# Performance work log

Measured on AMD Instinct MI355X. Metric: run time of the kernel, lower is better.

The kernel has to match this reference:

```python
import jax, jax.numpy as jnp
import numpy as np

EPS = 1e-12
B, S, H, NH, L, F = 8, 512, 768, 12, 12, 3072
V, TV, P = 21128, 2, 512
DH = H // NH


def layer_norm(x, g, b):
    m = jnp.mean(x, axis=-1, keepdims=True)
    v = jnp.var(x, axis=-1, keepdims=True)
    return g * (x - m) / jnp.sqrt(v + EPS) + b


def setup_inputs() -> dict:
    key = jax.random.key(0)
    ks = iter(jax.random.split(key, 40))
    r = lambda shape: (jax.random.normal(next(ks), shape, jnp.float32) * 0.02)
    inp = {
        "input_ids": jax.random.randint(next(ks), (B, S), 0, V, jnp.int32),
        "segment_ids": jax.random.randint(next(ks), (B, S), 0, TV, jnp.int32),
        "attention_mask": jnp.ones((B, 1, 1, S), jnp.float32),
        "tok_emb": r((V, H)),
        "pos_emb": r((P, H)),
        "type_emb": r((TV, H)),
        "emb_g": jnp.ones((H,), jnp.float32),
        "emb_b": jnp.zeros((H,), jnp.float32),
        # stacked per-layer params [L, ...]
        "Wq": r((L, H, H)), "bq": jnp.zeros((L, H), jnp.float32),
        "Wk": r((L, H, H)), "bk": jnp.zeros((L, H), jnp.float32),
        "Wv": r((L, H, H)), "bv": jnp.zeros((L, H), jnp.float32),
        "Wao": r((L, H, H)), "bao": jnp.zeros((L, H), jnp.float32),
        "ln1_g": jnp.ones((L, H), jnp.float32), "ln1_b": jnp.zeros((L, H), jnp.float32),
        "Wi": r((L, H, F)), "bi": jnp.zeros((L, F), jnp.float32),
        "Wio": r((L, F, H)), "bio": jnp.zeros((L, H), jnp.float32),
        "ln2_g": jnp.ones((L, H), jnp.float32), "ln2_b": jnp.zeros((L, H), jnp.float32),
    }
    return inp


def reference(input_ids, segment_ids, attention_mask,
              tok_emb, pos_emb, type_emb, emb_g, emb_b,
              Wq, bq, Wk, bk, Wv, bv, Wao, bao, ln1_g, ln1_b,
              Wi, bi, Wio, bio, ln2_g, ln2_b):
    # ---- embedding: token + type + position, then LayerNorm ----
    x = tok_emb[input_ids] + type_emb[segment_ids] + pos_emb[None, :S, :]
    x = layer_norm(x, emb_g, emb_b)  # [B,S,H]

    mask_add = (1.0 - attention_mask) * -10000.0  # [B,1,1,S]
    scale = 1.0 / jnp.sqrt(jnp.asarray(DH, x.dtype))

    def split_heads(t):  # [B,S,H] -> [B,NH,S,DH]
        return t.reshape(B, S, NH, DH).transpose(0, 2, 1, 3)

    for l in range(Wq.shape[0]):
        q = split_heads(x @ Wq[l] + bq[l])
        k = split_heads(x @ Wk[l] + bk[l])
        v = split_heads(x @ Wv[l] + bv[l])
        score = jnp.einsum("bhqd,bhkd->bhqk", q, k) * scale + mask_add
        attn = jax.nn.softmax(score, axis=-1)
        ctx = jnp.einsum("bhqk,bhkd->bhqd", attn, v)
        ctx = ctx.transpose(0, 2, 1, 3).reshape(B, S, H)
        # attention output: dense + residual + LN
        attn_out = layer_norm(ctx @ Wao[l] + bao[l] + x, ln1_g[l], ln1_b[l])
        # FFN: dense-gelu-dense + residual + LN (exact erf gelu as in tf.keras)
        h = jax.nn.gelu(attn_out @ Wi[l] + bi[l], approximate=False)
        x = layer_norm(h @ Wio[l] + bio[l] + attn_out, ln2_g[l], ln2_b[l])

    return x  # sequence output [B,S,H]
```

## Files before the change

kernel.cpp:

```cpp
#include <hip/hip_runtime.h>
#include <math.h>

static constexpr int Bc = 8;
static constexpr int Sc = 512;
static constexpr int Hc = 768;
static constexpr int NHc = 12;
static constexpr int Lc = 12;
static constexpr int Fc = 3072;
static constexpr int DHc = 64;
static constexpr int NTOK = Bc * Sc;
static constexpr int QKVN = 3 * Hc;

static constexpr size_t W_QKV_OFF = 0;
static constexpr size_t W_AO_OFF  = 1769472;
static constexpr size_t W_I_OFF   = 2359296;
static constexpr size_t W_IO_OFF  = 4718592;
static constexpr size_t LW        = 7077888;

typedef _Float16 h16x8 __attribute__((ext_vector_type(8)));
typedef float f32x4 __attribute__((ext_vector_type(4)));
typedef unsigned short us4 __attribute__((ext_vector_type(4)));
typedef unsigned short us8 __attribute__((ext_vector_type(8)));
typedef unsigned int u32x4 __attribute__((ext_vector_type(4)));

__device__ __forceinline__ unsigned short f2h(float f) {
    _Float16 h = (_Float16)f;
    return __builtin_bit_cast(unsigned short, h);
}
__device__ __forceinline__ float h2f(unsigned short u) {
    return (float)__builtin_bit_cast(_Float16, u);
}

#define AS1 __attribute__((address_space(1)))
#define AS3 __attribute__((address_space(3)))
__device__ __forceinline__ void gld_lds16(const void* g, void* l) {
    __builtin_amdgcn_global_load_lds((const AS1 void*)g, (AS3 void*)l, 16, 0, 0);
}

__global__ __launch_bounds__(256) void prep_kernel(
    const float* __restrict__ Wq, const float* __restrict__ Wk,
    const float* __restrict__ Wv, const float* __restrict__ Wao,
    const float* __restrict__ Wi, const float* __restrict__ Wio,
    const float* __restrict__ bq, const float* __restrict__ bk,
    const float* __restrict__ bv, unsigned short* __restrict__ WALL,
    float* __restrict__ BALL)
{
    int t = blockIdx.x, l = blockIdx.y;
    int tid = threadIdx.x;

    if (t >= 1728) {
        int idx = (t - 1728) * 256 + tid;
        float v = (idx < 768) ? bq[l * Hc + idx]
                : (idx < 1536) ? bk[l * Hc + idx - 768]
                               : bv[l * Hc + idx - 1536];
        BALL[(size_t)l * QKVN + idx] = v;
        return;
    }

    const float* src;
    unsigned short* dst;
    int K, N, ntn, local;
    if (t < 576) {
        int mat = t / 144; local = t % 144;
        K = 768; N = 768; ntn = 12;
        src = (mat == 0 ? Wq : mat == 1 ? Wk : mat == 2 ? Wv : Wao) + (size_t)l * 589824;
        dst = WALL + (size_t)l * LW + (mat < 3 ? (size_t)mat * 589824 : W_AO_OFF);
    } else if (t < 1152) {
        local = t - 576; K = 768; N = 3072; ntn = 48;
        src = Wi + (size_t)l * 2359296;
        dst = WALL + (size_t)l * LW + W_I_OFF;
    } else {
        local = t - 1152; K = 3072; N = 768; ntn = 12;
        src = Wio + (size_t)l * 2359296;
        dst = WALL + (size_t)l * LW + W_IO_OFF;
    }
    int n0 = (local % ntn) * 64, k0 = (local / ntn) * 64;

    int nkt = K >> 6;
    unsigned short* dstb = dst + ((size_t)(n0 >> 7) * nkt + (k0 >> 6)) * 8192
                               + ((n0 >> 6) & 1) * 4096;

    __shared__ float tl[64][65];
    int tx = tid & 15, ty = tid >> 4;
#pragma unroll
    for (int j = 0; j < 4; j++) {
        int k = ty + j * 16;
        float4 v = *(const float4*)(src + (size_t)(k0 + k) * N + n0 + tx * 4);
        tl[k][tx * 4 + 0] = v.x; tl[k][tx * 4 + 1] = v.y;
        tl[k][tx * 4 + 2] = v.z; tl[k][tx * 4 + 3] = v.w;
    }
    __syncthreads();
#pragma unroll
    for (int q = 0; q < 2; q++) {
        int chunk = q * 256 + tid;
        int row = chunk >> 3, c = chunk & 7;
        us8 o;
#pragma unroll
        for (int j = 0; j < 8; j++) o[j] = f2h(tl[c * 8 + j][row]);
        *(us8*)(dstb + (size_t)chunk * 8) = o;
    }
}

__device__ __forceinline__ void ln_stats192(float4 v, float& mean, float& rstd) {
    float s = v.x + v.y + v.z + v.w;
    float s2 = v.x * v.x + v.y * v.y + v.z * v.z + v.w * v.w;
#pragma unroll
    for (int o = 32; o > 0; o >>= 1) { s += __shfl_xor(s, o); s2 += __shfl_xor(s2, o); }
    __shared__ float red[6];
    int lane = threadIdx.x & 63, wid = threadIdx.x >> 6;
    if (lane == 0) { red[wid] = s; red[3 + wid] = s2; }
    __syncthreads();
    float ts  = red[0] + red[1] + red[2];
    float ts2 = red[3] + red[4] + red[5];
    mean = ts * (1.0f / Hc);
    float var = ts2 * (1.0f / Hc) - mean * mean;
    rstd = rsqrtf(var + 1e-12f);
}

__global__ __launch_bounds__(192) void embed_ln_kernel(
    const int* __restrict__ ids, const int* __restrict__ seg,
    const float* __restrict__ tok, const float* __restrict__ typ,
    const float* __restrict__ pos, const float* __restrict__ g,
    const float* __restrict__ b, unsigned short* __restrict__ outb)
{
    int t = blockIdx.x;
    int si = t % Sc;
    int id = ids[t], sg = seg[t];
    int i = threadIdx.x;

    float4 tv = *(const float4*)(tok + (size_t)id * Hc + 4 * i);
    float4 yv = *(const float4*)(typ + (size_t)sg * Hc + 4 * i);
    float4 pv = *(const float4*)(pos + (size_t)si * Hc + 4 * i);
    float4 v = make_float4(tv.x + yv.x + pv.x, tv.y + yv.y + pv.y,
                           tv.z + yv.z + pv.z, tv.w + yv.w + pv.w);
    float mean, rstd;
    ln_stats192(v, mean, rstd);

    float4 gv = *(const float4*)(g + 4 * i);
    float4 bv = *(const float4*)(b + 4 * i);
    us4 ob;
    ob[0] = f2h(gv.x * (v.x - mean) * rstd + bv.x);
    ob[1] = f2h(gv.y * (v.y - mean) * rstd + bv.y);
    ob[2] = f2h(gv.z * (v.z - mean) * rstd + bv.z);
    ob[3] = f2h(gv.w * (v.w - mean) * rstd + bv.w);
    *(us4*)(outb + (size_t)t * Hc + 4 * i) = ob;
}

__global__ __launch_bounds__(192) void add_ln2h_kernel(
    const unsigned short* __restrict__ t0, const unsigned short* __restrict__ t1,
    const unsigned short* __restrict__ res, const float* __restrict__ g,
    const float* __restrict__ b, unsigned short* __restrict__ outb,
    float* __restrict__ outf)
{
    int t = blockIdx.x;
    int i = threadIdx.x;
    us4 a = *(const us4*)(t0 + (size_t)t * Hc + 4 * i);
    us4 c = *(const us4*)(t1 + (size_t)t * Hc + 4 * i);
    us4 r = *(const us4*)(res + (size_t)t * Hc + 4 * i);
    float4 v = make_float4(h2f(a[0]) + h2f(c[0]) + h2f(r[0]),
                           h2f(a[1]) + h2f(c[1]) + h2f(r[1]),
                           h2f(a[2]) + h2f(c[2]) + h2f(r[2]),
                           h2f(a[3]) + h2f(c[3]) + h2f(r[3]));
    float mean, rstd;
    ln_stats192(v, mean, rstd);

    float4 gv = *(const float4*)(g + 4 * i);
    float4 bv = *(const float4*)(b + 4 * i);
    float4 o = make_float4(gv.x * (v.x - mean) * rstd + bv.x,
                           gv.y * (v.y - mean) * rstd + bv.y,
                           gv.z * (v.z - mean) * rstd + bv.z,
                           gv.w * (v.w - mean) * rstd + bv.w);
    us4 ob; ob[0] = f2h(o.x); ob[1] = f2h(o.y); ob[2] = f2h(o.z); ob[3] = f2h(o.w);
    *(us4*)(outb + (size_t)t * Hc + 4 * i) = ob;
    if (outf) *(float4*)(outf + (size_t)t * Hc + 4 * i) = o;
}

template <int OUT>
__global__ __launch_bounds__(256) void gemm_mfma(
    const unsigned short* __restrict__ A,
    const unsigned short* __restrict__ Bt,
    const float* __restrict__ bias,
    unsigned short* __restrict__ Cb,
    unsigned short* __restrict__ VTp,
    int M, int N, int K, int kspan)
{
    __shared__ __align__(16) unsigned short As[128 * 64];
    __shared__ __align__(16) unsigned short Bs[128 * 64];

    int tid = threadIdx.x;
    int l = tid & 63, w = tid >> 6;

    int nbx = gridDim.x;
    int nwg = nbx * gridDim.y;
    int bid = blockIdx.y * nbx + blockIdx.x;
    if ((nwg & 7) == 0) {
        int cpx = nwg >> 3;
        bid = (bid & 7) * cpx + (bid >> 3);
    }
    int m0 = (bid % nbx) * 128, n0 = (bid / nbx) * 128;

    int lr = l & 15;
    int kg = l >> 4;
    int wr = (w >> 1) * 64, wc = (w & 1) * 64;
    int lx = lr & 7;
    int kbeg = blockIdx.z * kspan;
    int nkt = K >> 6;
    const unsigned short* BtRow = Bt + (size_t)(n0 >> 7) * nkt * 8192;

    f32x4 acc[4][4] = {};

    for (int k0 = kbeg; k0 < kbeg + kspan; k0 += 64) {
        const unsigned short* gbBase = BtRow + (size_t)(k0 >> 6) * 8192;
#pragma unroll
        for (int p = 0; p < 4; p++) {
            int i = p * 256 + w * 64 + l;
            int row = i >> 3;
            int slot = (i & 7) ^ (row & 7);
            const unsigned short* ga = A + (size_t)(m0 + row) * K + k0 + slot * 8;
            const unsigned short* gb = gbBase + row * 64 + slot * 8;
            unsigned short* la = As + (size_t)(p * 256 + w * 64) * 8;
            unsigned short* lb = Bs + (size_t)(p * 256 + w * 64) * 8;
            gld_lds16(ga, la);
            gld_lds16(gb, lb);
        }
        asm volatile("s_waitcnt vmcnt(0)" ::: "memory");
        __syncthreads();

#pragma unroll
        for (int kh = 0; kh < 2; kh++) {
            h16x8 av[4], bv[4];
#pragma unroll
            for (int f = 0; f < 4; f++) {
                int sl = (kh * 4 + kg) ^ lx;
                av[f] = *(const h16x8*)(As + (wr + f * 16 + lr) * 64 + sl * 8);
                bv[f] = *(const h16x8*)(Bs + (wc + f * 16 + lr) * 64 + sl * 8);
            }
#pragma unroll
            for (int i = 0; i < 4; i++)
#pragma unroll
                for (int j = 0; j < 4; j++)
                    acc[i][j] = __builtin_amdgcn_mfma_f32_16x16x32_f16(
                        av[i], bv[j], acc[i][j], 0, 0, 0);
        }
        __syncthreads();
    }

#pragma unroll
    for (int i = 0; i < 4; i++) {
        int rbase = m0 + wr + i * 16 + kg * 4;
#pragma unroll
        for (int j = 0; j < 4; j++) {
            int col = n0 + wc + j * 16 + lr;
            float bcol = (OUT == 4 && blockIdx.z > 0) ? 0.f : bias[col];
            if (OUT == 3 && col >= 1536) {
                int vcol = col - 1536;
                int hh = vcol >> 6, d = vcol & 63;
                int bbb = rbase >> 9, s0 = rbase & 511;
                us4 ob;
#pragma unroll
                for (int r = 0; r < 4; r++) ob[r] = f2h(acc[i][j][r] + bcol);
                *(us4*)(VTp + ((((size_t)bbb * NHc + hh) * DHc + d) << 9) + s0) = ob;
            } else if (OUT == 4) {
                unsigned short* op = Cb + (size_t)blockIdx.z * M * N;
#pragma unroll
                for (int r = 0; r < 4; r++)
                    op[(size_t)(rbase + r) * N + col] = f2h(acc[i][j][r] + bcol);
            } else {
                int ldc = (OUT == 3) ? 1536 : N;
#pragma unroll
                for (int r = 0; r < 4; r++) {
                    float v = acc[i][j][r] + bcol;
                    if (OUT == 1) v = 0.5f * v * (1.0f + erff(v * 0.70710678118654752f));
                    Cb[(size_t)(rbase + r) * ldc + col] = f2h(v);
                }
            }
        }
    }
}

__global__ __launch_bounds__(512) void attn_mfma(
    const unsigned short* __restrict__ QK, const unsigned short* __restrict__ VT,
    const float* __restrict__ mask, unsigned short* __restrict__ O)
{
    const int LD = 1536;
    __shared__ __align__(16) unsigned short Ks[64 * 64];
    __shared__ __align__(16) unsigned short Vt[64 * 64];
    __shared__ float Ml[64];

    int tid = threadIdx.x;
    int l = tid & 63, w = tid >> 6;
    int g = l >> 4, c = l & 15;
    int q0 = blockIdx.x * 128;
    int h = blockIdx.y, bb = blockIdx.z;

    const size_t rowQ = (size_t)(bb * Sc + q0 + w * 16 + c) * LD + h * DHc;
    h16x8 qv[2];
    qv[0] = *(const h16x8*)(QK + rowQ + 8 * g);
    qv[1] = *(const h16x8*)(QK + rowQ + 32 + 8 * g);

    float m_run = -1e30f, l_run = 0.f;
    f32x4 acc_o[4] = {};
    const float scale = 0.125f;

    for (int kt = 0; kt < Sc; kt += 64) {
        const unsigned short* Kgb = QK + (size_t)(bb * Sc + kt) * LD + Hc + h * DHc;
        {
            int i = tid;
            int row = i >> 3;
            int slot = (i & 7) ^ (row & 7);
            gld_lds16(Kgb + (size_t)row * LD + slot * 8, Ks + (size_t)(w * 64) * 8);
        }
        const unsigned short* Vg = VT + (((size_t)bb * NHc + h) * DHc << 9) + kt;
        {
            int i = tid;
            int row = i >> 3;
            int slot = (i & 7) ^ (row & 7);
            gld_lds16(Vg + ((size_t)row << 9) + slot * 8, Vt + (size_t)(w * 64) * 8);
        }
        if (tid < 64) Ml[tid] = (1.0f - mask[bb * Sc + kt + tid]) * -10000.0f;
        asm volatile("s_waitcnt vmcnt(0)" ::: "memory");
        __syncthreads();

        f32x4 s[4] = {};
#pragma unroll
        for (int kh = 0; kh < 2; kh++) {
#pragma unroll
            for (int f = 0; f < 4; f++) {
                int row = f * 16 + c;
                h16x8 av = *(const h16x8*)(Ks + row * 64 + (((kh * 4 + g) ^ (row & 7)) * 8));
                s[f] = __builtin_amdgcn_mfma_f32_16x16x32_f16(av, qv[kh], s[f], 0, 0, 0);
            }
        }

        f32x4 mv[4];
#pragma unroll
        for (int f = 0; f < 4; f++) mv[f] = *(const f32x4*)&Ml[f * 16 + 4 * g];
        float mx = -1e30f;
#pragma unroll
        for (int f = 0; f < 4; f++)
#pragma unroll
            for (int r = 0; r < 4; r++) {
                float sv = s[f][r] * scale + mv[f][r];
                s[f][r] = sv;
                mx = fmaxf(mx, sv);
            }
        mx = fmaxf(mx, __shfl_xor(mx, 16));
        mx = fmaxf(mx, __shfl_xor(mx, 32));
        float mn = fmaxf(m_run, mx);
        float fs = __expf(m_run - mn);
        m_run = mn;
        float ps = 0.f;
        f32x4 p[4];
#pragma unroll
        for (int f = 0; f < 4; f++)
#pragma unroll
            for (int r = 0; r < 4; r++) {
                float pv = __expf(s[f][r] - mn);
                p[f][r] = pv;
                ps += pv;
            }
        ps += __shfl_xor(ps, 16);
        ps += __shfl_xor(ps, 32);
        l_run = l_run * fs + ps;
#pragma unroll
        for (int fm = 0; fm < 4; fm++)
#pragma unroll
            for (int r = 0; r < 4; r++) acc_o[fm][r] *= fs;

        unsigned pk[4][2];
#pragma unroll
        for (int f = 0; f < 4; f++)
#pragma unroll
            for (int rp = 0; rp < 2; rp++)
                pk[f][rp] = ((unsigned)f2h(p[f][2 * rp + 1]) << 16) | f2h(p[f][2 * rp]);

#pragma unroll
        for (int kh = 0; kh < 2; kh++) {
            u32x4 bw;
#pragma unroll
            for (int t = 0; t < 4; t++) {
                int srcl = (2 * ((l >> 4) & 1) + (t >> 1)) * 16 + c;
                unsigned lo = __shfl(pk[2 * kh][t & 1], srcl);
                unsigned hi = __shfl(pk[2 * kh + 1][t & 1], srcl);
                bw[t] = (g & 2) ? hi : lo;
            }
            h16x8 bfrag = __builtin_bit_cast(h16x8, bw);
#pragma unroll
            for (int fm = 0; fm < 4; fm++) {
                int row = fm * 16 + c;
                h16x8 av = *(const h16x8*)(Vt + row * 64 + (((kh * 4 + g) ^ (row & 7)) * 8));
                acc_o[fm] = __builtin_amdgcn_mfma_f32_16x16x32_f16(av, bfrag, acc_o[fm], 0, 0, 0);
            }
        }
        __syncthreads();
    }

    float rl = 1.0f / l_run;
    size_t tokrow = (size_t)(bb * Sc + q0 + w * 16 + c) * Hc + h * DHc;
#pragma unroll
    for (int fm = 0; fm < 4; fm++) {
        us4 ob;
#pragma unroll
        for (int r = 0; r < 4; r++) ob[r] = f2h(acc_o[fm][r] * rl);
        *(us4*)(O + tokrow + fm * 16 + 4 * g) = ob;
    }
}

extern "C" void kernel_launch(void* const* d_in, const int* in_sizes, int n_in,
                              void* d_out, int out_size, void* d_ws, size_t ws_size,
                              hipStream_t stream)
{
    const int*   input_ids      = (const int*)  d_in[0];
    const int*   segment_ids    = (const int*)  d_in[1];
    const float* attention_mask = (const float*)d_in[2];
    const float* tok_emb = (const float*)d_in[3];
    const float* pos_emb = (const float*)d_in[4];
    const float* type_emb= (const float*)d_in[5];
    const float* emb_g   = (const float*)d_in[6];
    const float* emb_b   = (const float*)d_in[7];
    const float* Wq  = (const float*)d_in[8];  const float* bq  = (const float*)d_in[9];
    const float* Wk  = (const float*)d_in[10]; const float* bk  = (const float*)d_in[11];
    const float* Wv  = (const float*)d_in[12]; const float* bv  = (const float*)d_in[13];
    const float* Wao = (const float*)d_in[14]; const float* bao = (const float*)d_in[15];
    const float* ln1_g = (const float*)d_in[16]; const float* ln1_b = (const float*)d_in[17];
    const float* Wi  = (const float*)d_in[18]; const float* bi  = (const float*)d_in[19];
    const float* Wio = (const float*)d_in[20]; const float* bio = (const float*)d_in[21];
    const float* ln2_g = (const float*)d_in[22]; const float* ln2_b = (const float*)d_in[23];

    float* out = (float*)d_out;

    const size_t NT = (size_t)NTOK * Hc;
    float* BALL = (float*)d_ws;
    unsigned short* QKb = (unsigned short*)(BALL + (size_t)Lc * QKVN);
    unsigned short* VT  = QKb + (size_t)NTOK * 1536;
    unsigned short* Xb  = VT + NT;
    unsigned short* XAb = Xb + NT;
    unsigned short* Cb  = XAb + NT;
    unsigned short* Tp  = Cb + NT;
    unsigned short* Hb  = Tp + 2 * NT;
    unsigned short* WALL = Hb + (size_t)NTOK * Fc;

    prep_kernel<<<dim3(1737, Lc), 256, 0, stream>>>(Wq, Wk, Wv, Wao, Wi, Wio,
                                                    bq, bk, bv, WALL, BALL);

    embed_ln_kernel<<<NTOK, 192, 0, stream>>>(input_ids, segment_ids, tok_emb,
                                              type_emb, pos_emb, emb_g, emb_b, Xb);

    dim3 gQKV(NTOK / 128, QKVN / 128);
    dim3 gF(NTOK / 128, Fc / 128);
    dim3 gH2(NTOK / 128, Hc / 128, 2);
    dim3 gA(Sc / 128, NHc, Bc);

    for (int l = 0; l < Lc; l++) {
        const unsigned short* WqkvT = WALL + (size_t)l * LW + W_QKV_OFF;
        const unsigned short* WaoT  = WALL + (size_t)l * LW + W_AO_OFF;
        const unsigned short* WiT   = WALL + (size_t)l * LW + W_I_OFF;
        const unsigned short* WioT  = WALL + (size_t)l * LW + W_IO_OFF;
        const float* bqkv = BALL + (size_t)l * QKVN;

        gemm_mfma<3><<<gQKV, 256, 0, stream>>>(Xb, WqkvT, bqkv, QKb, VT,
                                               NTOK, QKVN, Hc, Hc);
        attn_mfma<<<gA, 512, 0, stream>>>(QKb, VT, attention_mask, Cb);

        gemm_mfma<4><<<gH2, 256, 0, stream>>>(Cb, WaoT, bao + (size_t)l * Hc, Tp,
                                              nullptr, NTOK, Hc, Hc, Hc / 2);
        add_ln2h_kernel<<<NTOK, 192, 0, stream>>>(Tp, Tp + NT, Xb,
                                                  ln1_g + (size_t)l * Hc,
                                                  ln1_b + (size_t)l * Hc, XAb, nullptr);

        gemm_mfma<1><<<gF, 256, 0, stream>>>(XAb, WiT, bi + (size_t)l * Fc, Hb,
                                             nullptr, NTOK, Fc, Hc, Hc);
        gemm_mfma<4><<<gH2, 256, 0, stream>>>(Hb, WioT, bio + (size_t)l * Hc, Tp,
                                              nullptr, NTOK, Hc, Fc, Fc / 2);
        add_ln2h_kernel<<<NTOK, 192, 0, stream>>>(Tp, Tp + NT, XAb,
                                                  ln2_g + (size_t)l * Hc,
                                                  ln2_b + (size_t)l * Hc, Xb,
                                                  (l == Lc - 1) ? out : nullptr);
    }
}
```

Before: 1.950 ms.

## Stage GEMM epilogue through LDS for coalesced 16-byte stores; split prep per layer

The GEMM epilogue now writes bias-added (and GELU-applied) fp16 results into shared memory in two half-tile passes, then each thread stores contiguous 16-byte vectors to global memory. This replaces scattered 2-byte stores and aims to improve write coalescing, at the cost of extra LDS traffic and barriers. The V-transpose path for QKV is now selected per block. The weight-prep kernel is also launched once per layer instead of as a 2D grid, which adds launch overhead.

After: 2.347 ms. 1.2x slower.

```diff
diff --git a/kernel.cpp b/kernel.cpp
--- a/kernel.cpp
+++ b/kernel.cpp
@@ -43,9 +43,9 @@
     const float* __restrict__ Wi, const float* __restrict__ Wio,
     const float* __restrict__ bq, const float* __restrict__ bk,
     const float* __restrict__ bv, unsigned short* __restrict__ WALL,
-    float* __restrict__ BALL)
+    float* __restrict__ BALL, int l)
 {
-    int t = blockIdx.x, l = blockIdx.y;
+    int t = blockIdx.x;
     int tid = threadIdx.x;
 
     if (t >= 1728) {
@@ -184,8 +184,10 @@
     unsigned short* __restrict__ VTp,
     int M, int N, int K, int kspan)
 {
-    __shared__ __align__(16) unsigned short As[128 * 64];
-    __shared__ __align__(16) unsigned short Bs[128 * 64];
+    __shared__ __align__(16) unsigned short Smem[2 * 128 * 64];
+    unsigned short* As = Smem;
+    unsigned short* Bs = Smem + 128 * 64;
+    unsigned short* Cs = Smem;
 
     int tid = threadIdx.x;
     int l = tid & 63, w = tid >> 6;
@@ -245,14 +247,14 @@
         __syncthreads();
     }
 
-#pragma unroll
-    for (int i = 0; i < 4; i++) {
-        int rbase = m0 + wr + i * 16 + kg * 4;
-#pragma unroll
-        for (int j = 0; j < 4; j++) {
-            int col = n0 + wc + j * 16 + lr;
-            float bcol = (OUT == 4 && blockIdx.z > 0) ? 0.f : bias[col];
-            if (OUT == 3 && col >= 1536) {
+    if (OUT == 3 && n0 >= 1536) {
+#pragma unroll
+        for (int i = 0; i < 4; i++) {
+            int rbase = m0 + wr + i * 16 + kg * 4;
+#pragma unroll
+            for (int j = 0; j < 4; j++) {
+                int col = n0 + wc + j * 16 + lr;
+                float bcol = bias[col];
                 int vcol = col - 1536;
                 int hh = vcol >> 6, d = vcol & 63;
                 int bbb = rbase >> 9, s0 = rbase & 511;
@@ -260,20 +262,39 @@
 #pragma unroll
                 for (int r = 0; r < 4; r++) ob[r] = f2h(acc[i][j][r] + bcol);
                 *(us4*)(VTp + ((((size_t)bbb * NHc + hh) * DHc + d) << 9) + s0) = ob;
-            } else if (OUT == 4) {
-                unsigned short* op = Cb + (size_t)blockIdx.z * M * N;
-#pragma unroll
-                for (int r = 0; r < 4; r++)
-                    op[(size_t)(rbase + r) * N + col] = f2h(acc[i][j][r] + bcol);
-            } else {
-                int ldc = (OUT == 3) ? 1536 : N;
-#pragma unroll
-                for (int r = 0; r < 4; r++) {
-                    float v = acc[i][j][r] + bcol;
-                    if (OUT == 1) v = 0.5f * v * (1.0f + erff(v * 0.70710678118654752f));
-                    Cb[(size_t)(rbase + r) * ldc + col] = f2h(v);
-                }
-            }
+            }
+        }
+    } else {
+        const int ldc = (OUT == 3) ? 1536 : N;
+        unsigned short* outp = (OUT == 4) ? Cb + (size_t)blockIdx.z * M * N : Cb;
+#pragma unroll
+        for (int pass = 0; pass < 2; pass++) {
+            if ((w >> 1) == pass) {
+#pragma unroll
+                for (int i = 0; i < 4; i++)
+#pragma unroll
+                    for (int j = 0; j < 4; j++) {
+                        int col = wc + j * 16 + lr;
+                        float bcol = (OUT == 4 && blockIdx.z > 0) ? 0.f : bias[n0 + col];
+#pragma unroll
+                        for (int r = 0; r < 4; r++) {
+                            float v = acc[i][j][r] + bcol;
+                            if (OUT == 1)
+                                v = 0.5f * v * (1.0f + erff(v * 0.70710678118654752f));
+                            Cs[(i * 16 + kg * 4 + r) * 136 + col] = f2h(v);
+                        }
+                    }
+            }
+            __syncthreads();
+            {
+                int row = tid >> 2;
+                int c0 = (tid & 3) * 32;
+                unsigned short* gp = outp + (size_t)(m0 + pass * 64 + row) * ldc + n0 + c0;
+#pragma unroll
+                for (int q = 0; q < 4; q++)
+                    *(us8*)(gp + q * 8) = *(const us8*)(Cs + row * 136 + c0 + q * 8);
+            }
+            __syncthreads();
         }
     }
 }
@@ -440,8 +461,9 @@
     unsigned short* Hb  = Tp + 2 * NT;
     unsigned short* WALL = Hb + (size_t)NTOK * Fc;
 
-    prep_kernel<<<dim3(1737, Lc), 256, 0, stream>>>(Wq, Wk, Wv, Wao, Wi, Wio,
-                                                    bq, bk, bv, WALL, BALL);
+    for (int l = 0; l < Lc; l++)
+        prep_kernel<<<1737, 256, 0, stream>>>(Wq, Wk, Wv, Wao, Wi, Wio,
+                                              bq, bk, bv, WALL, BALL, l);
 
     embed_ln_kernel<<<NTOK, 192, 0, stream>>>(input_ids, segment_ids, tok_emb,
                                               type_emb, pos_emb, emb_g, emb_b, Xb);
```
